# Optimization experiments

Hardware: AMD Instinct MI355X
Metric: run time of the kernel (lower is better)

The kernel has to match this reference:

```python
import jax, jax.numpy as jnp
import numpy as np

B, S, D, DOUT = 8, 2048, 512, 512
BETA = 1.0
EPS = 1e-5


def _ln(x, g, b):
    m = jnp.mean(x, axis=-1, keepdims=True)
    v = jnp.var(x, axis=-1, keepdims=True)
    return (x - m) / jnp.sqrt(v + EPS) * g + b


def setup_inputs() -> dict:
    key = jax.random.key(0)
    ks = jax.random.split(key, 12)
    s = 0.02
    d = {
        "x": jax.random.normal(ks[0], (B, S, D), jnp.float32),
        "Wq": jax.random.normal(ks[1], (D, D), jnp.float32) * s,
        "bq": jnp.zeros((D,), jnp.float32),
        "Wk": jax.random.normal(ks[2], (D, D), jnp.float32) * s,
        "bk": jnp.zeros((D,), jnp.float32),
        "Wv": jax.random.normal(ks[3], (D, D), jnp.float32) * s,
        "bv": jnp.zeros((D,), jnp.float32),
        "ln0_g": jnp.ones((D,), jnp.float32),
        "ln0_b": jnp.zeros((D,), jnp.float32),
        "W1": jax.random.normal(ks[4], (D, D), jnp.float32) * s,
        "b1": jnp.zeros((D,), jnp.float32),
        "ln1_g": jnp.ones((D,), jnp.float32),
        "ln1_b": jnp.zeros((D,), jnp.float32),
        "W2": jax.random.normal(ks[5], (D, D), jnp.float32) * s,
        "b2": jnp.zeros((D,), jnp.float32),
        "ln2_g": jnp.ones((D,), jnp.float32),
        "ln2_b": jnp.zeros((D,), jnp.float32),
        "W3": jax.random.normal(ks[6], (D, DOUT), jnp.float32) * s,
        "b3": jnp.zeros((DOUT,), jnp.float32),
    }
    return d


def reference(x, Wq, bq, Wk, bk, Wv, bv, ln0_g, ln0_b,
              W1, b1, ln1_g, ln1_b, W2, b2, ln2_g, ln2_b, W3, b3):
    # --- attention_single (dropout disabled / eval) ---
    q = x @ Wq + bq                      # [B,S,D]
    k = x @ Wk + bk
    v = x @ Wv + bv
    scores = jnp.einsum('bsd,btd->bst', q, k)   # [B,S,S]
    w = jax.nn.softmax(BETA * scores / jnp.sqrt(jnp.float32(D)), axis=2)
    att = jnp.einsum('bst,btd->bsd', w, v)      # [B,S,D]
    out_nxt = _ln(x + att, ln0_g, ln0_b)
    # --- FFNN (dropout disabled, gelu activation) ---
    h1 = _ln(jax.nn.gelu(out_nxt + (out_nxt @ W1 + b1), approximate=False), ln1_g, ln1_b)
    h2 = _ln(jax.nn.gelu(out_nxt + (h1 @ W2 + b2), approximate=False), ln2_g, ln2_b)
    out_att = h2 @ W3 + b3               # [B,S,DOUT]
    return out_att
```

## Files before the change

### kernel.cpp

```cpp
#include <hip/hip_runtime.h>
#include <hip/hip_bf16.h>
#include <math.h>

using bf16 = __hip_bfloat16;
typedef __attribute__((ext_vector_type(8))) short short8;
typedef __attribute__((ext_vector_type(4))) float f32x4;
typedef __attribute__((ext_vector_type(4))) float float4v;
typedef __attribute__((ext_vector_type(4))) unsigned int uint4v;

__device__ __forceinline__ float b2f(bf16 v) { return __bfloat162float(v); }
__device__ __forceinline__ bf16 f2b(float v) { return __float2bfloat16(v); }

__device__ __forceinline__ unsigned char f2e4m3(float v) {
  int p = __builtin_amdgcn_cvt_pk_fp8_f32(v, v, 0, false);
  return (unsigned char)(p & 0xff);
}

__device__ __forceinline__ void gl_lds16(const void* g, void* l) {
  __builtin_amdgcn_global_load_lds(
      (const __attribute__((address_space(1))) void*)g,
      (__attribute__((address_space(3))) void*)l, 16, 0, 0);
}

__global__ __launch_bounds__(256) void sniff_zero(const void* ln0g_raw, int* flag,
                                                  float* rowsum) {
  const int i = blockIdx.x * 256 + threadIdx.x;
  rowsum[i] = 0.f;
  if (i == 0) {
    unsigned short w = ((const unsigned short*)ln0g_raw)[0];
    *flag = (w == 0x3F80) ? 1 : 0;
  }
}

__global__ __launch_bounds__(256) void conv_x8(
    const void* __restrict__ src, bf16* __restrict__ dst,
    const int* __restrict__ flag) {
  const long i = ((long)blockIdx.x * 256 + threadIdx.x) * 8;
  bf16 o[8];
  if (*flag) {
    *(short8*)(dst + i) = ((const short8*)src)[i >> 3];
  } else {
    float4v a = ((const float4v*)src)[i >> 2];
    float4v b = ((const float4v*)src)[(i >> 2) + 1];
#pragma unroll
    for (int k = 0; k < 4; k++) o[k] = f2b(a[k]);
#pragma unroll
    for (int k = 0; k < 4; k++) o[4 + k] = f2b(b[k]);
    *(short8*)(dst + i) = *(short8*)o;
  }
}

__global__ __launch_bounds__(256) void conv_vec12(
    const void* a0, const void* a1, const void* a2, const void* a3,
    const void* a4, const void* a5, const void* a6, const void* a7,
    const void* a8, const void* a9, const void* a10, const void* a11,
    bf16* __restrict__ dst, const int* __restrict__ flag) {
  const int j = blockIdx.x;
  const int i = threadIdx.x + (blockIdx.y << 8);
  const void* s;
  switch (j) {
    case 0: s = a0; break; case 1: s = a1; break; case 2: s = a2; break;
    case 3: s = a3; break; case 4: s = a4; break; case 5: s = a5; break;
    case 6: s = a6; break; case 7: s = a7; break; case 8: s = a8; break;
    case 9: s = a9; break; case 10: s = a10; break; default: s = a11; break;
  }
  bf16 v = (*flag) ? ((const bf16*)s)[i] : f2b(((const float*)s)[i]);
  dst[j * 512 + i] = v;
}

__global__ __launch_bounds__(256) void transpose_conv6(
    const void* w0, const void* w1, const void* w2, const void* w3,
    const void* w4, const void* w5, bf16* __restrict__ outBase,
    const int* __restrict__ flag) {
  __shared__ bf16 tile[32][33];
  const void* in;
  switch (blockIdx.z) {
    case 0: in = w0; break; case 1: in = w1; break; case 2: in = w2; break;
    case 3: in = w3; break; case 4: in = w4; break; default: in = w5; break;
  }
  bf16* out = outBase + (long)blockIdx.z * 262144;
  const int f = *flag;
  const int c0 = blockIdx.x * 32, r0 = blockIdx.y * 32;
  const int tx = threadIdx.x & 31, ty = threadIdx.x >> 5;
#pragma unroll
  for (int i = ty; i < 32; i += 8) {
    const long idx = (long)(r0 + i) * 512 + c0 + tx;
    tile[i][tx] = f ? ((const bf16*)in)[idx] : f2b(((const float*)in)[idx]);
  }
  __syncthreads();
#pragma unroll
  for (int i = ty; i < 32; i += 8)
    out[(long)(c0 + i) * 512 + r0 + tx] = tile[tx][i];
}


__global__ __launch_bounds__(256, 2) void gemm_scores(
    const bf16* __restrict__ A, const bf16* __restrict__ Bt,
    unsigned char* __restrict__ out8, float* __restrict__ rowsum,
    int N, int K, long sA, long sB, long sC, float scale) {
  __shared__ __align__(16) bf16 As[2][128 * 64];
  __shared__ __align__(16) bf16 Bs[2][128 * 64];
  const int z = blockIdx.x;
  const int m0 = blockIdx.y * 128, n0 = blockIdx.z * 128;
  A += (long)z * sA;
  Bt += (long)z * sB;
  const int t = threadIdx.x;
  const int l = t & 63, w = t >> 6;
  const int wm = (w >> 1) * 64, wn = (w & 1) * 64;
  const int lr = l & 15, lq = l >> 4;

  const bf16* Ab = A + (long)m0 * K;
  const bf16* Bb = Bt + (long)n0 * K;

  int srcoff[4];
#pragma unroll
  for (int reg = 0; reg < 4; reg++) {
    const int s = reg * 256 + t;
    const int row = s >> 3, pch = s & 7;
    const int L = pch ^ (row & 7);
    srcoff[reg] = row * K + L * 8;
  }

  f32x4 acc[4][4] = {};

#pragma unroll
  for (int reg = 0; reg < 4; reg++) {
    gl_lds16(Ab + srcoff[reg], &As[0][reg * 2048 + w * 512]);
    gl_lds16(Bb + srcoff[reg], &Bs[0][reg * 2048 + w * 512]);
  }

  const int nkt = K >> 6;
  for (int kt = 0; kt < nkt; kt++) {
    const int cur = kt & 1;
    if (kt + 1 < nkt) {
      const int k0n = (kt + 1) << 6;
#pragma unroll
      for (int reg = 0; reg < 4; reg++) {
        gl_lds16(Ab + srcoff[reg] + k0n, &As[cur ^ 1][reg * 2048 + w * 512]);
        gl_lds16(Bb + srcoff[reg] + k0n, &Bs[cur ^ 1][reg * 2048 + w * 512]);
      }
      asm volatile("s_waitcnt vmcnt(8)" ::: "memory");
    } else {
      asm volatile("s_waitcnt vmcnt(0)" ::: "memory");
    }
    __builtin_amdgcn_s_barrier();
    const bf16* Asl = As[cur];
    const bf16* Bsl = Bs[cur];
#pragma unroll
    for (int kh = 0; kh < 2; kh++) {
      short8 af[4], bfr[4];
#pragma unroll
      for (int i = 0; i < 4; i++) {
        const int r = wm + i * 16 + lr;
        const int pc = (kh * 4 + lq) ^ (r & 7);
        af[i] = *(const short8*)(Asl + r * 64 + pc * 8);
      }
#pragma unroll
      for (int j = 0; j < 4; j++) {
        const int r = wn + j * 16 + lr;
        const int pc = (kh * 4 + lq) ^ (r & 7);
        bfr[j] = *(const short8*)(Bsl + r * 64 + pc * 8);
      }
#pragma unroll
      for (int i = 0; i < 4; i++)
#pragma unroll
        for (int j = 0; j < 4; j++)
          acc[i][j] = __builtin_amdgcn_mfma_f32_16x16x32_bf16(af[i], bfr[j], acc[i][j], 0, 0, 0);
    }
    __builtin_amdgcn_s_barrier();
  }

  const int cr = lq * 4, cc = lr;
  unsigned char* tile = (unsigned char*)&As[0][0];
  float rs[4][4] = {};
#pragma unroll
  for (int i = 0; i < 4; i++) {
#pragma unroll
    for (int j = 0; j < 4; j++) {
#pragma unroll
      for (int r = 0; r < 4; r++) {
        float e = __expf(acc[i][j][r] * scale);
        tile[(wm + i * 16 + cr + r) * 132 + wn + j * 16 + cc] = f2e4m3(e);
        rs[i][r] += e;
      }
    }
  }
#pragma unroll
  for (int o = 1; o < 16; o <<= 1)
#pragma unroll
    for (int i = 0; i < 4; i++)
#pragma unroll
      for (int r = 0; r < 4; r++) rs[i][r] += __shfl_xor(rs[i][r], o);
  if (lr == 0) {
#pragma unroll
    for (int i = 0; i < 4; i++)
#pragma unroll
      for (int r = 0; r < 4; r++) {
        const int gr = m0 + wm + i * 16 + cr + r;
        atomicAdd(&rowsum[(long)z * 2048 + gr], rs[i][r]);
      }
  }
  __syncthreads();
  const long obase = (long)z * sC + (long)m0 * N + n0;
#pragma unroll
  for (int its = 0; its < 4; its++) {
    const int row = its * 32 + (t >> 3);
    const int ch = (t & 7) * 16;
    const unsigned int* sp = (const unsigned int*)(tile + row * 132 + ch);
    uint4v v = {sp[0], sp[1], sp[2], sp[3]};
    *(uint4v*)(out8 + obase + (long)row * N + ch) = v;
  }
}

template <int EPI, bool BX>
__global__ __launch_bounds__(256, 2) void gemm_sk(
    const bf16* __restrict__ A, const bf16* __restrict__ Bt,
    const bf16* __restrict__ bias, const bf16* __restrict__ res,
    float* __restrict__ outF, bf16* __restrict__ outB,
    unsigned char* __restrict__ out8,
    int M, int N, int K, long sA, long sB, long sC, long sBias) {
  __shared__ __align__(16) bf16 As[64 * 64];
  __shared__ __align__(16) bf16 Bs[128 * 64];
  const int z = BX ? blockIdx.x : blockIdx.z;
  const int m0 = (BX ? blockIdx.y : blockIdx.x) * 64;
  const int n0 = (BX ? blockIdx.z : blockIdx.y) * 128;
  A += (long)z * sA;
  Bt += (long)z * sB;
  if (EPI == 0) bias += (long)z * sBias;
  const int t = threadIdx.x;
  const int l = t & 63, w = t >> 6;
  const int wm = (w >> 1) * 32, wn = (w & 1) * 64;
  const int lr = l & 15, lq = l >> 4;

  const bf16* Ab = A + (long)m0 * K;
  const bf16* Bb = Bt + (long)n0 * K;

  int srcoff[4];
#pragma unroll
  for (int reg = 0; reg < 4; reg++) {
    const int s = reg * 256 + t;
    const int row = s >> 3, pch = s & 7;
    const int L = pch ^ (row & 7);
    srcoff[reg] = row * K + L * 8;
  }

  f32x4 acc[2][4] = {};

  for (int k0 = 0; k0 < K; k0 += 64) {
    gl_lds16(Ab + srcoff[0] + k0, As + w * 512);
    gl_lds16(Ab + srcoff[1] + k0, As + 2048 + w * 512);
#pragma unroll
    for (int reg = 0; reg < 4; reg++)
      gl_lds16(Bb + srcoff[reg] + k0, Bs + reg * 2048 + w * 512);
    __syncthreads();
#pragma unroll
    for (int kh = 0; kh < 2; kh++) {
      short8 af[2], bfr[4];
#pragma unroll
      for (int i = 0; i < 2; i++) {
        const int r = wm + i * 16 + lr;
        const int pc = (kh * 4 + lq) ^ (r & 7);
        af[i] = *(const short8*)(As + r * 64 + pc * 8);
      }
#pragma unroll
      for (int j = 0; j < 4; j++) {
        const int r = wn + j * 16 + lr;
        const int pc = (kh * 4 + lq) ^ (r & 7);
        bfr[j] = *(const short8*)(Bs + r * 64 + pc * 8);
      }
#pragma unroll
      for (int i = 0; i < 2; i++)
#pragma unroll
        for (int j = 0; j < 4; j++)
          acc[i][j] = __builtin_amdgcn_mfma_f32_16x16x32_bf16(af[i], bfr[j], acc[i][j], 0, 0, 0);
    }
    __syncthreads();
  }

  const int cr = lq * 4, cc = lr;
  if (EPI == 6) {
    unsigned char* tile = (unsigned char*)Bs;
#pragma unroll
    for (int i = 0; i < 2; i++) {
#pragma unroll
      for (int j = 0; j < 4; j++) {
#pragma unroll
        for (int r = 0; r < 4; r++) {
          const int gr = m0 + wm + i * 16 + cr + r;
          float v = acc[i][j][r] + b2f(bias[gr]);
          tile[(wm + i * 16 + cr + r) * 132 + wn + j * 16 + cc] = f2e4m3(v);
        }
      }
    }
    __syncthreads();
    const long obase = (long)z * sC + (long)m0 * N + n0;
#pragma unroll
    for (int its = 0; its < 2; its++) {
      const int row = its * 32 + (t >> 3);
      const int ch = (t & 7) * 16;
      const unsigned int* sp = (const unsigned int*)(tile + row * 132 + ch);
      uint4v v = {sp[0], sp[1], sp[2], sp[3]};
      *(uint4v*)(out8 + obase + (long)row * N + ch) = v;
    }
    return;
  }
#pragma unroll
  for (int i = 0; i < 2; i++) {
#pragma unroll
    for (int j = 0; j < 4; j++) {
      const int gc = n0 + wn + j * 16 + cc;
#pragma unroll
      for (int r = 0; r < 4; r++) {
        const int gr = m0 + wm + i * 16 + cr + r;
        const long idx = (long)z * sC + (long)gr * N + gc;
        float v = acc[i][j][r];
        if (EPI == 0) {
          v += b2f(bias[gc]);
          outB[idx] = f2b(v);
        } else if (EPI == 3) {
          v += b2f(bias[gc]) + b2f(res[idx]);
          v = 0.5f * v * (1.0f + erff(v * 0.70710678118654752f));
          outB[idx] = f2b(v);
        } else {
          v += b2f(bias[gc]);
          outF[idx] = v;
        }
      }
    }
  }
}

__global__ __launch_bounds__(256, 2) void gemm_pv8(
    const unsigned char* __restrict__ A8, const unsigned char* __restrict__ B8,
    const bf16* __restrict__ res, bf16* __restrict__ outB,
    const float* __restrict__ rowsum,
    int M, int N, int K, long sA, long sB, long sC) {
  __shared__ __align__(16) unsigned char As8[128 * 64];
  __shared__ __align__(16) unsigned char Bs8[128 * 64];
  const int z = blockIdx.x;
  const int m0 = blockIdx.y * 128, n0 = blockIdx.z * 128;
  A8 += (long)z * sA;
  B8 += (long)z * sB;
  const int t = threadIdx.x;
  const int l = t & 63, w = t >> 6;
  const int wm = (w >> 1) * 64, wn = (w & 1) * 64;
  const int lr = l & 15, lq = l >> 4;

  const unsigned char* Ab = A8 + (long)m0 * K;
  const unsigned char* Bb = B8 + (long)n0 * K;

  int soff[2];
#pragma unroll
  for (int reg = 0; reg < 2; reg++) {
    const int s = reg * 256 + t;
    const int row = s >> 2, pch = s & 3;
    const int L = pch ^ ((row >> 1) & 3);
    soff[reg] = row * K + L * 16;
  }

  f32x4 acc[4][4] = {};

  for (int k0 = 0; k0 < K; k0 += 64) {
#pragma unroll
    for (int reg = 0; reg < 2; reg++) {
      gl_lds16(Ab + soff[reg] + k0, As8 + reg * 4096 + w * 1024);
      gl_lds16(Bb + soff[reg] + k0, Bs8 + reg * 4096 + w * 1024);
    }
    __syncthreads();
#pragma unroll
    for (int kh = 0; kh < 2; kh++) {
      long long a8[4], b8[4];
#pragma unroll
      for (int i = 0; i < 4; i++) {
        const int ar = wm + i * 16 + lr;
        const int Lx = (kh * 2 + (lq >> 1)) ^ ((ar >> 1) & 3);
        a8[i] = *(const long long*)(As8 + ar * 64 + Lx * 16 + (lq & 1) * 8);
      }
#pragma unroll
      for (int j = 0; j < 4; j++) {
        const int br = wn + j * 16 + lr;
        const int Lx = (kh * 2 + (lq >> 1)) ^ ((br >> 1) & 3);
        b8[j] = *(const long long*)(Bs8 + br * 64 + Lx * 16 + (lq & 1) * 8);
      }
#pragma unroll
      for (int i = 0; i < 4; i++)
#pragma unroll
        for (int j = 0; j < 4; j++)
          acc[i][j] = __builtin_amdgcn_mfma_f32_16x16x32_fp8_fp8(a8[i], b8[j], acc[i][j], 0, 0, 0);
    }
    __syncthreads();
  }

  const int cr = lq * 4, cc = lr;
  float inv[4][4];
#pragma unroll
  for (int i = 0; i < 4; i++)
#pragma unroll
    for (int r = 0; r < 4; r++) {
      const int gr = m0 + wm + i * 16 + cr + r;
      inv[i][r] = 1.0f / rowsum[(long)z * 2048 + gr];
    }
#pragma unroll
  for (int i = 0; i < 4; i++) {
#pragma unroll
    for (int j = 0; j < 4; j++) {
      const int gc = n0 + wn + j * 16 + cc;
#pragma unroll
      for (int r = 0; r < 4; r++) {
        const int gr = m0 + wm + i * 16 + cr + r;
        const long idx = (long)z * sC + (long)gr * N + gc;
        float v = acc[i][j][r] * inv[i][r] + b2f(res[idx]);
        outB[idx] = f2b(v);
      }
    }
  }
}

__global__ __launch_bounds__(256) void ln512(
    const bf16* __restrict__ mainb,
    const bf16* __restrict__ g, const bf16* __restrict__ b,
    bf16* __restrict__ out) {
  const int t = threadIdx.x;
  const int l = t & 63, w = t >> 6;
  const long row = (long)blockIdx.x * 4 + w;
  const long base = row * 512 + l * 8;
  bf16 vb8[8];
  *(short8*)vb8 = *(const short8*)(mainb + base);
  float v[8];
  float s = 0.f, q = 0.f;
#pragma unroll
  for (int k = 0; k < 8; k++) {
    v[k] = b2f(vb8[k]);
    s += v[k];
    q += v[k] * v[k];
  }
#pragma unroll
  for (int o = 32; o > 0; o >>= 1) {
    s += __shfl_xor(s, o);
    q += __shfl_xor(q, o);
  }
  const float mean = s * (1.f / 512.f);
  const float var = q * (1.f / 512.f) - mean * mean;
  const float rstd = rsqrtf(var + 1e-5f);
  bf16 g8[8], b8[8], o8[8];
  *(short8*)g8 = *(const short8*)(g + l * 8);
  *(short8*)b8 = *(const short8*)(b + l * 8);
#pragma unroll
  for (int k = 0; k < 8; k++)
    o8[k] = f2b((v[k] - mean) * rstd * b2f(g8[k]) + b2f(b8[k]));
  *(short8*)(out + base) = *(short8*)o8;
}

__global__ void sentinel_kernel(float* out) { out[0] = 31337.0f; }

extern "C" void kernel_launch(void* const* d_in, const int* in_sizes, int n_in,
                              void* d_out, int out_size, void* d_ws, size_t ws_size,
                              hipStream_t stream) {
  const void* x_raw = d_in[0];
  const void* Wq = d_in[1];
  const void* bq = d_in[2];
  const void* Wk = d_in[3];
  const void* bk = d_in[4];
  const void* Wv = d_in[5];
  const void* bv = d_in[6];
  const void* ln0g = d_in[7];
  const void* ln0b = d_in[8];
  const void* W1 = d_in[9];
  const void* b1 = d_in[10];
  const void* ln1g = d_in[11];
  const void* ln1b = d_in[12];
  const void* W2 = d_in[13];
  const void* b2 = d_in[14];
  const void* ln2g = d_in[15];
  const void* ln2b = d_in[16];
  const void* W3 = d_in[17];
  const void* b3 = d_in[18];

  const long MB = 1024 * 1024;
  if (ws_size < (size_t)(148 * MB)) {
    sentinel_kernel<<<1, 1, 0, stream>>>((float*)d_out);
    return;
  }
  char* ws = (char*)d_ws;
  bf16* Wqt = (bf16*)(ws + 0L * 524288);
  bf16* Wvt = (bf16*)(ws + 2L * 524288);
  bf16* W1t = (bf16*)(ws + 3L * 524288);
  bf16* W2t = (bf16*)(ws + 4L * 524288);
  bf16* W3t = (bf16*)(ws + 5L * 524288);
  int* flag = (int*)(ws + 3 * MB);
  bf16* vec = (bf16*)(ws + 3 * MB + 1024);
  bf16* bqc = vec + 0 * 512;
  bf16* bvc = vec + 2 * 512;
  bf16* ln0gc = vec + 3 * 512;
  bf16* ln0bc = vec + 4 * 512;
  bf16* b1c = vec + 5 * 512;
  bf16* ln1gc = vec + 6 * 512;
  bf16* ln1bc = vec + 7 * 512;
  bf16* b2c = vec + 8 * 512;
  bf16* ln2gc = vec + 9 * 512;
  bf16* ln2bc = vec + 10 * 512;
  bf16* b3c = vec + 11 * 512;
  float* rowsum = (float*)(ws + 3 * MB + 131072);
  bf16* xc = (bf16*)(ws + 4 * MB);
  bf16* qb = (bf16*)(ws + 20 * MB);
  bf16* kb = (bf16*)(ws + 36 * MB);
  unsigned char* vt8 = (unsigned char*)(ws + 52 * MB);
  unsigned char* sc8 = (unsigned char*)(ws + 68 * MB);
  bf16* sres = (bf16*)(ws + 132 * MB);
  bf16* onx = (bf16*)(ws + 20 * MB);
  bf16* preh = (bf16*)(ws + 68 * MB);
  bf16* h1 = (bf16*)(ws + 36 * MB);
  bf16* h2 = (bf16*)(ws + 100 * MB);

  const dim3 blk(256);
  const float scale = 0.044194173824159216f;
  const long sQ = 2048L * 512, sS = 2048L * 2048;

  sniff_zero<<<dim3(64), blk, 0, stream>>>(ln0g, flag, rowsum);
  conv_x8<<<dim3(4096), blk, 0, stream>>>(x_raw, xc, flag);
  conv_vec12<<<dim3(12, 2), blk, 0, stream>>>(bq, bk, bv, ln0g, ln0b, b1, ln1g,
                                              ln1b, b2, ln2g, ln2b, b3, vec, flag);
  transpose_conv6<<<dim3(16, 16, 6), blk, 0, stream>>>(Wq, Wk, Wv, W1, W2, W3,
                                                       Wqt, flag);

  gemm_sk<0, false><<<dim3(256, 4, 2), blk, 0, stream>>>(
      xc, Wqt, bqc, nullptr, nullptr, qb, nullptr,
      16384, 512, 512, 0, 262144, 8388608, 512);
  gemm_sk<6, true><<<dim3(8, 8, 16), blk, 0, stream>>>(
      Wvt, xc, bvc, nullptr, nullptr, nullptr, vt8,
      512, 2048, 512, 0, sQ, sQ, 0);
  gemm_scores<<<dim3(8, 16, 16), blk, 0, stream>>>(
      qb, kb, sc8, rowsum, 2048, 512, sQ, sQ, sS, scale);
  gemm_pv8<<<dim3(8, 16, 4), blk, 0, stream>>>(
      sc8, vt8, xc, sres, rowsum, 2048, 512, 2048, sS, sQ, sQ);
  ln512<<<dim3(4096), blk, 0, stream>>>(sres, ln0gc, ln0bc, onx);
  gemm_sk<3, false><<<dim3(256, 4, 1), blk, 0, stream>>>(
      onx, W1t, b1c, onx, nullptr, preh, nullptr,
      16384, 512, 512, 0, 0, 0, 0);
  ln512<<<dim3(4096), blk, 0, stream>>>(preh, ln1gc, ln1bc, h1);
  gemm_sk<3, false><<<dim3(256, 4, 1), blk, 0, stream>>>(
      h1, W2t, b2c, onx, nullptr, preh, nullptr,
      16384, 512, 512, 0, 0, 0, 0);
  ln512<<<dim3(4096), blk, 0, stream>>>(preh, ln2gc, ln2bc, h2);
  gemm_sk<4, false><<<dim3(256, 4, 1), blk, 0, stream>>>(
      h2, W3t, b3c, nullptr, (float*)d_out, nullptr, nullptr,
      16384, 512, 512, 0, 0, 0, 0);
}
```

Measured before the change: 344.8 us.

## Grow projection/FFN GEMM tiles to 128x128 and drop score GEMM double buffering

```diff
diff --git a/kernel.cpp b/kernel.cpp
--- a/kernel.cpp
+++ b/kernel.cpp
@@ -98,8 +98,9 @@
     const bf16* __restrict__ A, const bf16* __restrict__ Bt,
     unsigned char* __restrict__ out8, float* __restrict__ rowsum,
     int N, int K, long sA, long sB, long sC, float scale) {
-  __shared__ __align__(16) bf16 As[2][128 * 64];
-  __shared__ __align__(16) bf16 Bs[2][128 * 64];
+  __shared__ __align__(16) bf16 smem[2 * 128 * 64];
+  bf16* As = smem;
+  bf16* Bs = smem + 8192;
   const int z = blockIdx.x;
   const int m0 = blockIdx.y * 128, n0 = blockIdx.z * 128;
   A += (long)z * sA;
@@ -123,29 +124,13 @@
 
   f32x4 acc[4][4] = {};
 
-#pragma unroll
-  for (int reg = 0; reg < 4; reg++) {
-    gl_lds16(Ab + srcoff[reg], &As[0][reg * 2048 + w * 512]);
-    gl_lds16(Bb + srcoff[reg], &Bs[0][reg * 2048 + w * 512]);
-  }
-
-  const int nkt = K >> 6;
-  for (int kt = 0; kt < nkt; kt++) {
-    const int cur = kt & 1;
-    if (kt + 1 < nkt) {
-      const int k0n = (kt + 1) << 6;
-#pragma unroll
-      for (int reg = 0; reg < 4; reg++) {
-        gl_lds16(Ab + srcoff[reg] + k0n, &As[cur ^ 1][reg * 2048 + w * 512]);
-        gl_lds16(Bb + srcoff[reg] + k0n, &Bs[cur ^ 1][reg * 2048 + w * 512]);
-      }
-      asm volatile("s_waitcnt vmcnt(8)" ::: "memory");
-    } else {
-      asm volatile("s_waitcnt vmcnt(0)" ::: "memory");
-    }
-    __builtin_amdgcn_s_barrier();
-    const bf16* Asl = As[cur];
-    const bf16* Bsl = Bs[cur];
+  for (int k0 = 0; k0 < K; k0 += 64) {
+#pragma unroll
+    for (int reg = 0; reg < 4; reg++) {
+      gl_lds16(Ab + srcoff[reg] + k0, As + reg * 2048 + w * 512);
+      gl_lds16(Bb + srcoff[reg] + k0, Bs + reg * 2048 + w * 512);
+    }
+    __syncthreads();
 #pragma unroll
     for (int kh = 0; kh < 2; kh++) {
       short8 af[4], bfr[4];
@@ -153,13 +138,13 @@
       for (int i = 0; i < 4; i++) {
         const int r = wm + i * 16 + lr;
         const int pc = (kh * 4 + lq) ^ (r & 7);
-        af[i] = *(const short8*)(Asl + r * 64 + pc * 8);
+        af[i] = *(const short8*)(As + r * 64 + pc * 8);
       }
 #pragma unroll
       for (int j = 0; j < 4; j++) {
         const int r = wn + j * 16 + lr;
         const int pc = (kh * 4 + lq) ^ (r & 7);
-        bfr[j] = *(const short8*)(Bsl + r * 64 + pc * 8);
+        bfr[j] = *(const short8*)(Bs + r * 64 + pc * 8);
       }
 #pragma unroll
       for (int i = 0; i < 4; i++)
@@ -167,11 +152,11 @@
         for (int j = 0; j < 4; j++)
           acc[i][j] = __builtin_amdgcn_mfma_f32_16x16x32_bf16(af[i], bfr[j], acc[i][j], 0, 0, 0);
     }
-    __builtin_amdgcn_s_barrier();
+    __syncthreads();
   }
 
   const int cr = lq * 4, cc = lr;
-  unsigned char* tile = (unsigned char*)&As[0][0];
+  unsigned char* tile = (unsigned char*)smem;
   float rs[4][4] = {};
 #pragma unroll
   for (int i = 0; i < 4; i++) {
@@ -213,23 +198,24 @@
 }
 
 template <int EPI, bool BX>
-__global__ __launch_bounds__(256, 2) void gemm_sk(
+__global__ __launch_bounds__(256, 2) void gemm128(
     const bf16* __restrict__ A, const bf16* __restrict__ Bt,
     const bf16* __restrict__ bias, const bf16* __restrict__ res,
     float* __restrict__ outF, bf16* __restrict__ outB,
     unsigned char* __restrict__ out8,
-    int M, int N, int K, long sA, long sB, long sC, long sBias) {
-  __shared__ __align__(16) bf16 As[64 * 64];
-  __shared__ __align__(16) bf16 Bs[128 * 64];
+    int N, int K, long sA, long sB, long sC, long sBias) {
+  __shared__ __align__(16) bf16 smem[2 * 128 * 64];
+  bf16* As = smem;
+  bf16* Bs = smem + 8192;
   const int z = BX ? blockIdx.x : blockIdx.z;
-  const int m0 = (BX ? blockIdx.y : blockIdx.x) * 64;
+  const int m0 = (BX ? blockIdx.y : blockIdx.x) * 128;
   const int n0 = (BX ? blockIdx.z : blockIdx.y) * 128;
   A += (long)z * sA;
   Bt += (long)z * sB;
   if (EPI == 0) bias += (long)z * sBias;
   const int t = threadIdx.x;
   const int l = t & 63, w = t >> 6;
-  const int wm = (w >> 1) * 32, wn = (w & 1) * 64;
+  const int wm = (w >> 1) * 64, wn = (w & 1) * 64;
   const int lr = l & 15, lq = l >> 4;
 
   const bf16* Ab = A + (long)m0 * K;
@@ -244,20 +230,20 @@
     srcoff[reg] = row * K + L * 8;
   }
 
-  f32x4 acc[2][4] = {};
+  f32x4 acc[4][4] = {};
 
   for (int k0 = 0; k0 < K; k0 += 64) {
-    gl_lds16(Ab + srcoff[0] + k0, As + w * 512);
-    gl_lds16(Ab + srcoff[1] + k0, As + 2048 + w * 512);
-#pragma unroll
-    for (int reg = 0; reg < 4; reg++)
+#pragma unroll
+    for (int reg = 0; reg < 4; reg++) {
+      gl_lds16(Ab + srcoff[reg] + k0, As + reg * 2048 + w * 512);
       gl_lds16(Bb + srcoff[reg] + k0, Bs + reg * 2048 + w * 512);
+    }
     __syncthreads();
 #pragma unroll
     for (int kh = 0; kh < 2; kh++) {
-      short8 af[2], bfr[4];
-#pragma unroll
-      for (int i = 0; i < 2; i++) {
+      short8 af[4], bfr[4];
+#pragma unroll
+      for (int i = 0; i < 4; i++) {
         const int r = wm + i * 16 + lr;
         const int pc = (kh * 4 + lq) ^ (r & 7);
         af[i] = *(const short8*)(As + r * 64 + pc * 8);
@@ -269,7 +255,7 @@
         bfr[j] = *(const short8*)(Bs + r * 64 + pc * 8);
       }
 #pragma unroll
-      for (int i = 0; i < 2; i++)
+      for (int i = 0; i < 4; i++)
 #pragma unroll
         for (int j = 0; j < 4; j++)
           acc[i][j] = __builtin_amdgcn_mfma_f32_16x16x32_bf16(af[i], bfr[j], acc[i][j], 0, 0, 0);
@@ -279,9 +265,9 @@
 
   const int cr = lq * 4, cc = lr;
   if (EPI == 6) {
-    unsigned char* tile = (unsigned char*)Bs;
-#pragma unroll
-    for (int i = 0; i < 2; i++) {
+    unsigned char* tile = (unsigned char*)smem;
+#pragma unroll
+    for (int i = 0; i < 4; i++) {
 #pragma unroll
       for (int j = 0; j < 4; j++) {
 #pragma unroll
@@ -295,7 +281,7 @@
     __syncthreads();
     const long obase = (long)z * sC + (long)m0 * N + n0;
 #pragma unroll
-    for (int its = 0; its < 2; its++) {
+    for (int its = 0; its < 4; its++) {
       const int row = its * 32 + (t >> 3);
       const int ch = (t & 7) * 16;
       const unsigned int* sp = (const unsigned int*)(tile + row * 132 + ch);
@@ -305,7 +291,7 @@
     return;
   }
 #pragma unroll
-  for (int i = 0; i < 2; i++) {
+  for (int i = 0; i < 4; i++) {
 #pragma unroll
     for (int j = 0; j < 4; j++) {
       const int gc = n0 + wn + j * 16 + cc;
@@ -523,26 +509,26 @@
   transpose_conv6<<<dim3(16, 16, 6), blk, 0, stream>>>(Wq, Wk, Wv, W1, W2, W3,
                                                        Wqt, flag);
 
-  gemm_sk<0, false><<<dim3(256, 4, 2), blk, 0, stream>>>(
+  gemm128<0, false><<<dim3(128, 4, 2), blk, 0, stream>>>(
       xc, Wqt, bqc, nullptr, nullptr, qb, nullptr,
-      16384, 512, 512, 0, 262144, 8388608, 512);
-  gemm_sk<6, true><<<dim3(8, 8, 16), blk, 0, stream>>>(
+      512, 512, 0, 262144, 8388608, 512);
+  gemm128<6, true><<<dim3(8, 4, 16), blk, 0, stream>>>(
       Wvt, xc, bvc, nullptr, nullptr, nullptr, vt8,
-      512, 2048, 512, 0, sQ, sQ, 0);
+      2048, 512, 0, sQ, sQ, 0);
   gemm_scores<<<dim3(8, 16, 16), blk, 0, stream>>>(
       qb, kb, sc8, rowsum, 2048, 512, sQ, sQ, sS, scale);
   gemm_pv8<<<dim3(8, 16, 4), blk, 0, stream>>>(
       sc8, vt8, xc, sres, rowsum, 2048, 512, 2048, sS, sQ, sQ);
   ln512<<<dim3(4096), blk, 0, stream>>>(sres, ln0gc, ln0bc, onx);
-  gemm_sk<3, false><<<dim3(256, 4, 1), blk, 0, stream>>>(
+  gemm128<3, false><<<dim3(128, 4, 1), blk, 0, stream>>>(
       onx, W1t, b1c, onx, nullptr, preh, nullptr,
-      16384, 512, 512, 0, 0, 0, 0);
+      512, 512, 0, 0, 0, 0);
   ln512<<<dim3(4096), blk, 0, stream>>>(preh, ln1gc, ln1bc, h1);
-  gemm_sk<3, false><<<dim3(256, 4, 1), blk, 0, stream>>>(
+  gemm128<3, false><<<dim3(128, 4, 1), blk, 0, stream>>>(
       h1, W2t, b2c, onx, nullptr, preh, nullptr,
-      16384, 512, 512, 0, 0, 0, 0);
+      512, 512, 0, 0, 0, 0);
   ln512<<<dim3(4096), blk, 0, stream>>>(preh, ln2gc, ln2bc, h2);
-  gemm_sk<4, false><<<dim3(256, 4, 1), blk, 0, stream>>>(
+  gemm128<4, false><<<dim3(128, 4, 1), blk, 0, stream>>>(
       h2, W3t, b3c, nullptr, (float*)d_out, nullptr, nullptr,
-      16384, 512, 512, 0, 0, 0, 0);
-}
+      512, 512, 0, 0, 0, 0);
+}
```

After: 330.6 us. -4.1%, faster.
